# Optimization experiments

Measured on AMD Instinct MI355X. Metric: run time of the kernel, lower is better.

## Reference

```python
import jax, jax.numpy as jnp
import numpy as np

INPUT_SIZE, HIDDEN_SIZE, OUTPUT_SIZE = 64, 256, 1


def setup_inputs() -> dict:
    key = jax.random.key(0)
    ks = jax.random.split(key, 7)
    B, T, I, H, O = 256, 512, INPUT_SIZE, HIDDEN_SIZE, OUTPUT_SIZE
    s_ih = 1.0 / np.sqrt(H)
    return {
        "x": jax.random.normal(ks[0], (B, T, I), dtype=jnp.float32),
        # PyTorch GRUCell layout: rows ordered [reset, update, new], shape [3H, in]
        "w_ih": jax.random.uniform(ks[1], (3 * H, I), jnp.float32, -s_ih, s_ih),
        "w_hh": jax.random.uniform(ks[2], (3 * H, H), jnp.float32, -s_ih, s_ih),
        "b_ih": jax.random.uniform(ks[3], (3 * H,), jnp.float32, -s_ih, s_ih),
        "b_hh": jax.random.uniform(ks[4], (3 * H,), jnp.float32, -s_ih, s_ih),
        "w_out": jax.random.uniform(ks[5], (O, H), jnp.float32, -s_ih, s_ih),
        "b_out": jax.random.uniform(ks[6], (O,), jnp.float32, -s_ih, s_ih),
    }


def reference(x, w_ih, w_hh, b_ih, b_hh, w_out, b_out):
    B, T, I = x.shape
    H = w_hh.shape[1]
    # Precompute all input-side gate projections in one big GEMM: [T, B, 3H]
    gi_all = jnp.einsum("bti,gi->tbg", x, w_ih) + b_ih

    def step(h, gi):
        gh = h @ w_hh.T + b_hh  # [B, 3H]
        i_r, i_z, i_n = jnp.split(gi, 3, axis=-1)
        h_r, h_z, h_n = jnp.split(gh, 3, axis=-1)
        r = jax.nn.sigmoid(i_r + h_r)
        z = jax.nn.sigmoid(i_z + h_z)
        n = jnp.tanh(i_n + r * h_n)
        h_new = (1.0 - z) * n + z * h
        return h_new, h_new

    h0 = jnp.zeros((B, H), dtype=x.dtype)
    _, hs = jax.lax.scan(step, h0, gi_all)  # hs: [T, B, H]
    outs = jnp.einsum("tbh,oh->tbo", hs, w_out) + b_out  # [T, B, O]
    return outs
```

## Files before the change

kernel.cpp:

```cpp
#include <hip/hip_runtime.h>

typedef _Float16 half8 __attribute__((ext_vector_type(8)));
typedef _Float16 f16x2 __attribute__((ext_vector_type(2)));
typedef float floatx4 __attribute__((ext_vector_type(4)));

#define NB 256
#define NT 512
#define NI 64
#define NH 256
#define NSEQ 16
#define NBLK (NB / NSEQ)
#define THR 1024
#define HS 344

#define WB_N (480 * 512)

__global__ __launch_bounds__(256) void gru_prep_kernel(
    const float* __restrict__ w_ih, const float* __restrict__ w_hh,
    _Float16* __restrict__ wb)
{
  int n = blockIdx.x * 256 + threadIdx.x;
  if (n >= WB_N) return;
  int i = n & 7, l = (n >> 3) & 63, f = n >> 9;
  int q = l >> 4, col = l & 15;
  int tt, kb, gate;
  if (f < 160)      { tt = f / 10;               kb = f % 10;        gate = 0; }
  else if (f < 320) { int f2 = f - 160; tt = f2 / 10; kb = f2 % 10;  gate = 1; }
  else if (f < 448) { int f3 = f - 320; tt = f3 / 8;  kb = f3 % 8;   gate = 2; }
  else              { int f4 = f - 448; tt = f4 / 2;  kb = 8 + (f4 & 1); gate = 3; }
  int j = (tt & 15) * 16 + col;
  int k = kb * 32 + q * 8 + i;
  float v;
  if (gate == 0)      v = (k < 256) ? w_hh[(0   + j) * 256 + k] : w_ih[(0   + j) * 64 + (k - 256)];
  else if (gate == 1) v = (k < 256) ? w_hh[(256 + j) * 256 + k] : w_ih[(256 + j) * 64 + (k - 256)];
  else if (gate == 2) v = w_hh[(512 + j) * 256 + k];
  else                v = w_ih[(512 + j) * 64 + (k - 256)];
  wb[n] = (_Float16)v;
}

__device__ __forceinline__ float sigm(float v) {
  return __builtin_amdgcn_rcpf(1.0f + __expf(-v));
}
__device__ __forceinline__ float tanh_f(float v) {
  return 1.0f - 2.0f * __builtin_amdgcn_rcpf(1.0f + __expf(2.0f * v));
}

#define MFMA16(a, b, c) __builtin_amdgcn_mfma_f32_16x16x32_f16(a, b, c, 0, 0, 0)
#define FDOT(W, X, A) __builtin_amdgcn_fdot2(__builtin_bit_cast(f16x2, W), \
                                             __builtin_bit_cast(f16x2, X), A, false)

__global__ __launch_bounds__(THR) void gru_kernel(
    const float* __restrict__ x,
    const float* __restrict__ b_ih,
    const float* __restrict__ b_hh,
    const _Float16* __restrict__ wb,
    _Float16* __restrict__ HD,
    float* __restrict__ out)
{
  __shared__ __align__(16) _Float16 H[2][NSEQ][HS];
  __shared__ __align__(16) _Float16 WN[8 * 16 * 512];

  const int tid  = threadIdx.x;
  const int lane = tid & 63;
  const int w    = tid >> 6;
  const int q    = lane >> 4;
  const int col  = lane & 15;
  const int b0   = blockIdx.x * NSEQ;
  const int j    = w * 16 + col;

  {
    const float4* src = (const float4*)(wb + (size_t)320 * 512);
    float4* dst = (float4*)WN;
    #pragma unroll
    for (int it = 0; it < 8; ++it) dst[tid + it * THR] = src[tid + it * THR];
  }

  const _Float16* wbL = wb + (size_t)lane * 8;
#define LBR(k) const half8 BR##k = *(const half8*)(wbL + (size_t)(w * 10 + (k)) * 512);
  LBR(0) LBR(1) LBR(2) LBR(3) LBR(4) LBR(5) LBR(6) LBR(7) LBR(8) LBR(9)
#undef LBR
#define LBZ(k) const half8 BZ##k = *(const half8*)(wbL + (size_t)(160 + w * 10 + (k)) * 512);
  LBZ(0) LBZ(1) LBZ(2) LBZ(3) LBZ(4) LBZ(5)
#undef LBZ
  const half8* sZ6 = (const half8*)(wbL + (size_t)(160 + w * 10 + 6) * 512);
  const half8* sZ7 = (const half8*)(wbL + (size_t)(160 + w * 10 + 7) * 512);
  const half8* sZ8 = (const half8*)(wbL + (size_t)(160 + w * 10 + 8) * 512);
  const half8* sZ9 = (const half8*)(wbL + (size_t)(160 + w * 10 + 9) * 512);
  const half8* sI0 = (const half8*)(wbL + (size_t)(448 + w * 2 + 0) * 512);
  const half8* sI1 = (const half8*)(wbL + (size_t)(448 + w * 2 + 1) * 512);

  const float br   = b_ih[j] + b_hh[j];
  const float bz   = b_ih[256 + j] + b_hh[256 + j];
  const float bin_ = b_ih[512 + j];
  const float bhn  = b_hh[512 + j];

  {
    float4* hz = (float4*)H;
    #pragma unroll
    for (int it = 0; it < 2; ++it) {
      int idx = tid + it * THR;
      if (idx < (int)(sizeof(H) / 16)) hz[idx] = float4{0, 0, 0, 0};
    }
  }
  __syncthreads();
  H[0][tid >> 6][256 + (tid & 63)] =
      (_Float16)x[(size_t)(b0 + (tid >> 6)) * (NT * NI) + (tid & 63)];
  float h0 = 0.0f, h1 = 0.0f, h2 = 0.0f, h3 = 0.0f;
  const float* xp = x + (size_t)(b0 + (tid >> 6)) * (NT * NI) + 64 + (tid & 63);
  __syncthreads();

  for (int t = 0; t < NT; ++t) {
    const int cur = t & 1, nxt = cur ^ 1;
    half8 SZ6 = *sZ6, SZ7 = *sZ7, SZ8 = *sZ8, SZ9 = *sZ9, SI0i = *sI0, SI1i = *sI1;
    float xv = 0.0f;
    if (t + 1 < NT) xv = xp[(size_t)t * 64];

    if (t > 0 && tid < 512) {
      int row = tid >> 5, ch = tid & 31;
      float4 hv = *(const float4*)&H[cur][row][ch * 8];
      *(float4*)(HD + ((size_t)(t - 1) * NB + b0 + row) * NH + ch * 8) = hv;
    }

    const _Float16* hrow = &H[cur][col][q * 8];
    floatx4 cR = {0, 0, 0, 0}, cZ = {0, 0, 0, 0}, cN = {0, 0, 0, 0}, cI = {0, 0, 0, 0};
#define KBN(k, BZk) { \
    half8 a = *(const half8*)(hrow + (k) * 32); \
    cR = MFMA16(a, BR##k, cR); \
    cZ = MFMA16(a, BZk, cZ); \
    cN = MFMA16(a, *(const half8*)&WN[(w * 8 + (k)) * 512 + lane * 8], cN); }
    KBN(0, BZ0) KBN(1, BZ1) KBN(2, BZ2) KBN(3, BZ3) KBN(4, BZ4) KBN(5, BZ5)
    KBN(6, SZ6) KBN(7, SZ7)
#undef KBN
    { half8 a = *(const half8*)(hrow + 8 * 32);
      cR = MFMA16(a, BR8, cR); cZ = MFMA16(a, SZ8, cZ); cI = MFMA16(a, SI0i, cI); }
    { half8 a = *(const half8*)(hrow + 9 * 32);
      cR = MFMA16(a, BR9, cR); cZ = MFMA16(a, SZ9, cZ); cI = MFMA16(a, SI1i, cI); }

#define GATE(m, hvar) { \
    float rr = sigm(cR[m] + br); \
    float zz = sigm(cZ[m] + bz); \
    float nn = tanh_f(cI[m] + bin_ + rr * (cN[m] + bhn)); \
    hvar = (1.0f - zz) * nn + zz * hvar; \
    H[nxt][q * 4 + (m)][j] = (_Float16)hvar; }
    GATE(0, h0) GATE(1, h1) GATE(2, h2) GATE(3, h3)
#undef GATE
    if (t + 1 < NT) H[nxt][tid >> 6][256 + (tid & 63)] = (_Float16)xv;

    __syncthreads();
  }

  if (tid < 512) {
    int row = tid >> 5, ch = tid & 31;
    float4 hv = *(const float4*)&H[0][row][ch * 8];
    *(float4*)(HD + ((size_t)(NT - 1) * NB + b0 + row) * NH + ch * 8) = hv;
  }
}

__global__ __launch_bounds__(256) void gru_out_kernel(
    const _Float16* __restrict__ HD, const float* __restrict__ w_out,
    const float* __restrict__ b_out, float* __restrict__ out)
{
  __shared__ __align__(16) _Float16 WL[NH];
  int tid = threadIdx.x;
  WL[tid] = (_Float16)w_out[tid];
  __syncthreads();
  int gid = blockIdx.x * 256 + tid;
  const float4* hp = (const float4*)(HD + (size_t)gid * NH);
  const float4* wp = (const float4*)WL;
  float acc = 0.0f;
  #pragma unroll
  for (int i = 0; i < NH / 8; ++i) {
    float4 hv = hp[i];
    float4 wv = wp[i];
    acc = FDOT(hv.x, wv.x, acc);
    acc = FDOT(hv.y, wv.y, acc);
    acc = FDOT(hv.z, wv.z, acc);
    acc = FDOT(hv.w, wv.w, acc);
  }
  out[gid] = acc + b_out[0];
}

extern "C" void kernel_launch(void* const* d_in, const int* in_sizes, int n_in,
                              void* d_out, int out_size, void* d_ws, size_t ws_size,
                              hipStream_t stream) {
  const float* x     = (const float*)d_in[0];
  const float* w_ih  = (const float*)d_in[1];
  const float* w_hh  = (const float*)d_in[2];
  const float* b_ih  = (const float*)d_in[3];
  const float* b_hh  = (const float*)d_in[4];
  const float* w_out = (const float*)d_in[5];
  const float* b_out = (const float*)d_in[6];
  float* out = (float*)d_out;

  _Float16* wb = (_Float16*)d_ws;
  _Float16* HD = wb + WB_N;

  gru_prep_kernel<<<(WB_N + 255) / 256, 256, 0, stream>>>(w_ih, w_hh, wb);
  gru_kernel<<<NBLK, THR, 0, stream>>>(x, b_ih, b_hh, wb, HD, out);
  gru_out_kernel<<<(NT * NB) / 256, 256, 0, stream>>>(HD, w_out, b_out, out);
}
```

Measured before the change: 1.247 ms.

## Halve GRU block to 512 threads, two hidden tiles per wave

Each block now runs 8 waves instead of 16, and each wave computes two 16-column hidden tiles. The R and Z weights for both tiles are held in registers. The N-gate weights are no longer kept in shared memory; they are streamed from global memory each step, with loads interleaved between the MFMA groups and an asm barrier that stops the compiler hoisting them. The aim is to use one A-fragment read from shared memory for twice as many MFMAs and to spend less per step on block barriers, at the cost of much higher register pressure and repeated global or L2 weight loads on every timestep.

```diff
diff --git a/kernel.cpp b/kernel.cpp
--- a/kernel.cpp
+++ b/kernel.cpp
@@ -10,7 +10,7 @@
 #define NH 256
 #define NSEQ 16
 #define NBLK (NB / NSEQ)
-#define THR 1024
+#define THR 512
 #define HS 344
 
 #define WB_N (480 * 512)
@@ -49,7 +49,7 @@
 #define FDOT(W, X, A) __builtin_amdgcn_fdot2(__builtin_bit_cast(f16x2, W), \
                                              __builtin_bit_cast(f16x2, X), A, false)
 
-__global__ __launch_bounds__(THR) void gru_kernel(
+__global__ __launch_bounds__(THR, 2) void gru_kernel(
     const float* __restrict__ x,
     const float* __restrict__ b_ih,
     const float* __restrict__ b_hh,
@@ -58,7 +58,6 @@
     float* __restrict__ out)
 {
   __shared__ __align__(16) _Float16 H[2][NSEQ][HS];
-  __shared__ __align__(16) _Float16 WN[8 * 16 * 512];
 
   const int tid  = threadIdx.x;
   const int lane = tid & 63;
@@ -66,90 +65,123 @@
   const int q    = lane >> 4;
   const int col  = lane & 15;
   const int b0   = blockIdx.x * NSEQ;
-  const int j    = w * 16 + col;
-
-  {
-    const float4* src = (const float4*)(wb + (size_t)320 * 512);
-    float4* dst = (float4*)WN;
-    #pragma unroll
-    for (int it = 0; it < 8; ++it) dst[tid + it * THR] = src[tid + it * THR];
-  }
+  const int t0   = 2 * w;
+  const int t1   = 2 * w + 1;
+  const int j0   = t0 * 16 + col;
+  const int j1   = t1 * 16 + col;
 
   const _Float16* wbL = wb + (size_t)lane * 8;
-#define LBR(k) const half8 BR##k = *(const half8*)(wbL + (size_t)(w * 10 + (k)) * 512);
-  LBR(0) LBR(1) LBR(2) LBR(3) LBR(4) LBR(5) LBR(6) LBR(7) LBR(8) LBR(9)
-#undef LBR
-#define LBZ(k) const half8 BZ##k = *(const half8*)(wbL + (size_t)(160 + w * 10 + (k)) * 512);
-  LBZ(0) LBZ(1) LBZ(2) LBZ(3) LBZ(4) LBZ(5)
-#undef LBZ
-  const half8* sZ6 = (const half8*)(wbL + (size_t)(160 + w * 10 + 6) * 512);
-  const half8* sZ7 = (const half8*)(wbL + (size_t)(160 + w * 10 + 7) * 512);
-  const half8* sZ8 = (const half8*)(wbL + (size_t)(160 + w * 10 + 8) * 512);
-  const half8* sZ9 = (const half8*)(wbL + (size_t)(160 + w * 10 + 9) * 512);
-  const half8* sI0 = (const half8*)(wbL + (size_t)(448 + w * 2 + 0) * 512);
-  const half8* sI1 = (const half8*)(wbL + (size_t)(448 + w * 2 + 1) * 512);
-
-  const float br   = b_ih[j] + b_hh[j];
-  const float bz   = b_ih[256 + j] + b_hh[256 + j];
-  const float bin_ = b_ih[512 + j];
-  const float bhn  = b_hh[512 + j];
+
+#define LR(T, k) const half8 R##T##_##k = *(const half8*)(wbL + (size_t)(t##T * 10 + (k)) * 512);
+  LR(0,0) LR(0,1) LR(0,2) LR(0,3) LR(0,4) LR(0,5) LR(0,6) LR(0,7) LR(0,8) LR(0,9)
+  LR(1,0) LR(1,1) LR(1,2) LR(1,3) LR(1,4) LR(1,5) LR(1,6) LR(1,7) LR(1,8) LR(1,9)
+#undef LR
+#define LZ(T, k) const half8 Z##T##_##k = *(const half8*)(wbL + (size_t)(160 + t##T * 10 + (k)) * 512);
+  LZ(0,0) LZ(0,1) LZ(0,2) LZ(0,3) LZ(0,4) LZ(0,5) LZ(0,6) LZ(0,7) LZ(0,8) LZ(0,9)
+  LZ(1,0) LZ(1,1) LZ(1,2) LZ(1,3) LZ(1,4) LZ(1,5) LZ(1,6) LZ(1,7) LZ(1,8) LZ(1,9)
+#undef LZ
+
+  uintptr_t pN0 = (uintptr_t)(wbL + (size_t)(320 + t0 * 8) * 512);
+  uintptr_t pN1 = (uintptr_t)(wbL + (size_t)(320 + t1 * 8) * 512);
+  uintptr_t pI0 = (uintptr_t)(wbL + (size_t)(448 + t0 * 2) * 512);
+  uintptr_t pI1 = (uintptr_t)(wbL + (size_t)(448 + t1 * 2) * 512);
+
+  const float br0  = b_ih[j0] + b_hh[j0];
+  const float bz0  = b_ih[256 + j0] + b_hh[256 + j0];
+  const float bin0 = b_ih[512 + j0];
+  const float bhn0 = b_hh[512 + j0];
+  const float br1  = b_ih[j1] + b_hh[j1];
+  const float bz1  = b_ih[256 + j1] + b_hh[256 + j1];
+  const float bin1 = b_ih[512 + j1];
+  const float bhn1 = b_hh[512 + j1];
 
   {
     float4* hz = (float4*)H;
     #pragma unroll
-    for (int it = 0; it < 2; ++it) {
+    for (int it = 0; it < 3; ++it) {
       int idx = tid + it * THR;
       if (idx < (int)(sizeof(H) / 16)) hz[idx] = float4{0, 0, 0, 0};
     }
   }
   __syncthreads();
-  H[0][tid >> 6][256 + (tid & 63)] =
-      (_Float16)x[(size_t)(b0 + (tid >> 6)) * (NT * NI) + (tid & 63)];
-  float h0 = 0.0f, h1 = 0.0f, h2 = 0.0f, h3 = 0.0f;
-  const float* xp = x + (size_t)(b0 + (tid >> 6)) * (NT * NI) + 64 + (tid & 63);
+  H[0][w][256 + lane]     = (_Float16)x[(size_t)(b0 + w)     * (NT * NI) + lane];
+  H[0][w + 8][256 + lane] = (_Float16)x[(size_t)(b0 + w + 8) * (NT * NI) + lane];
+  float h00 = 0.0f, h01 = 0.0f, h02 = 0.0f, h03 = 0.0f;
+  float h10 = 0.0f, h11 = 0.0f, h12 = 0.0f, h13 = 0.0f;
+  const float* xp0 = x + (size_t)(b0 + w)     * (NT * NI) + 64 + lane;
+  const float* xp1 = x + (size_t)(b0 + w + 8) * (NT * NI) + 64 + lane;
   __syncthreads();
 
   for (int t = 0; t < NT; ++t) {
     const int cur = t & 1, nxt = cur ^ 1;
-    half8 SZ6 = *sZ6, SZ7 = *sZ7, SZ8 = *sZ8, SZ9 = *sZ9, SI0i = *sI0, SI1i = *sI1;
-    float xv = 0.0f;
-    if (t + 1 < NT) xv = xp[(size_t)t * 64];
-
-    if (t > 0 && tid < 512) {
+    asm("" : "+v"(pN0), "+v"(pN1), "+v"(pI0), "+v"(pI1));
+    const half8* sN0 = (const half8*)pN0;
+    const half8* sN1 = (const half8*)pN1;
+    const half8* sI0 = (const half8*)pI0;
+    const half8* sI1 = (const half8*)pI1;
+
+    half8 sa0 = sN0[0 * 64], sb0 = sN1[0 * 64];
+    half8 sa1 = sN0[1 * 64], sb1 = sN1[1 * 64];
+    half8 sa2 = sN0[2 * 64], sb2 = sN1[2 * 64];
+    float xv0 = 0.0f, xv1 = 0.0f;
+    if (t + 1 < NT) { xv0 = xp0[(size_t)t * 64]; xv1 = xp1[(size_t)t * 64]; }
+
+    if (t > 0) {
       int row = tid >> 5, ch = tid & 31;
       float4 hv = *(const float4*)&H[cur][row][ch * 8];
       *(float4*)(HD + ((size_t)(t - 1) * NB + b0 + row) * NH + ch * 8) = hv;
     }
 
     const _Float16* hrow = &H[cur][col][q * 8];
-    floatx4 cR = {0, 0, 0, 0}, cZ = {0, 0, 0, 0}, cN = {0, 0, 0, 0}, cI = {0, 0, 0, 0};
-#define KBN(k, BZk) { \
+    floatx4 cR0 = {0, 0, 0, 0}, cZ0 = {0, 0, 0, 0}, cN0 = {0, 0, 0, 0}, cI0 = {0, 0, 0, 0};
+    floatx4 cR1 = {0, 0, 0, 0}, cZ1 = {0, 0, 0, 0}, cN1 = {0, 0, 0, 0}, cI1 = {0, 0, 0, 0};
+#define KGRP(k, NA, NB_) { \
     half8 a = *(const half8*)(hrow + (k) * 32); \
-    cR = MFMA16(a, BR##k, cR); \
-    cZ = MFMA16(a, BZk, cZ); \
-    cN = MFMA16(a, *(const half8*)&WN[(w * 8 + (k)) * 512 + lane * 8], cN); }
-    KBN(0, BZ0) KBN(1, BZ1) KBN(2, BZ2) KBN(3, BZ3) KBN(4, BZ4) KBN(5, BZ5)
-    KBN(6, SZ6) KBN(7, SZ7)
-#undef KBN
+    cR0 = MFMA16(a, R0_##k, cR0); cR1 = MFMA16(a, R1_##k, cR1); \
+    cZ0 = MFMA16(a, Z0_##k, cZ0); cZ1 = MFMA16(a, Z1_##k, cZ1); \
+    cN0 = MFMA16(a, NA, cN0);     cN1 = MFMA16(a, NB_, cN1); }
+    KGRP(0, sa0, sb0)  half8 sa3 = sN0[3 * 64], sb3 = sN1[3 * 64];
+    KGRP(1, sa1, sb1)  half8 sa4 = sN0[4 * 64], sb4 = sN1[4 * 64];
+    KGRP(2, sa2, sb2)  half8 sa5 = sN0[5 * 64], sb5 = sN1[5 * 64];
+    KGRP(3, sa3, sb3)  half8 sa6 = sN0[6 * 64], sb6 = sN1[6 * 64];
+    KGRP(4, sa4, sb4)  half8 sa7 = sN0[7 * 64], sb7 = sN1[7 * 64];
+    KGRP(5, sa5, sb5)  half8 ia0 = sI0[0],      ib0 = sI1[0];
+    KGRP(6, sa6, sb6)  half8 ia1 = sI0[64],     ib1 = sI1[64];
+    KGRP(7, sa7, sb7)
+#undef KGRP
     { half8 a = *(const half8*)(hrow + 8 * 32);
-      cR = MFMA16(a, BR8, cR); cZ = MFMA16(a, SZ8, cZ); cI = MFMA16(a, SI0i, cI); }
+      cR0 = MFMA16(a, R0_8, cR0); cR1 = MFMA16(a, R1_8, cR1);
+      cZ0 = MFMA16(a, Z0_8, cZ0); cZ1 = MFMA16(a, Z1_8, cZ1);
+      cI0 = MFMA16(a, ia0, cI0);  cI1 = MFMA16(a, ib0, cI1); }
     { half8 a = *(const half8*)(hrow + 9 * 32);
-      cR = MFMA16(a, BR9, cR); cZ = MFMA16(a, SZ9, cZ); cI = MFMA16(a, SI1i, cI); }
-
-#define GATE(m, hvar) { \
-    float rr = sigm(cR[m] + br); \
-    float zz = sigm(cZ[m] + bz); \
-    float nn = tanh_f(cI[m] + bin_ + rr * (cN[m] + bhn)); \
+      cR0 = MFMA16(a, R0_9, cR0); cR1 = MFMA16(a, R1_9, cR1);
+      cZ0 = MFMA16(a, Z0_9, cZ0); cZ1 = MFMA16(a, Z1_9, cZ1);
+      cI0 = MFMA16(a, ia1, cI0);  cI1 = MFMA16(a, ib1, cI1); }
+
+#define GATE(m, hvar, CR, CZ, CN, CI, BR_, BZ_, BI_, BH_, J) { \
+    float rr = sigm(CR[m] + BR_); \
+    float zz = sigm(CZ[m] + BZ_); \
+    float nn = tanh_f(CI[m] + BI_ + rr * (CN[m] + BH_)); \
     hvar = (1.0f - zz) * nn + zz * hvar; \
-    H[nxt][q * 4 + (m)][j] = (_Float16)hvar; }
-    GATE(0, h0) GATE(1, h1) GATE(2, h2) GATE(3, h3)
+    H[nxt][q * 4 + (m)][J] = (_Float16)hvar; }
+    GATE(0, h00, cR0, cZ0, cN0, cI0, br0, bz0, bin0, bhn0, j0)
+    GATE(1, h01, cR0, cZ0, cN0, cI0, br0, bz0, bin0, bhn0, j0)
+    GATE(2, h02, cR0, cZ0, cN0, cI0, br0, bz0, bin0, bhn0, j0)
+    GATE(3, h03, cR0, cZ0, cN0, cI0, br0, bz0, bin0, bhn0, j0)
+    GATE(0, h10, cR1, cZ1, cN1, cI1, br1, bz1, bin1, bhn1, j1)
+    GATE(1, h11, cR1, cZ1, cN1, cI1, br1, bz1, bin1, bhn1, j1)
+    GATE(2, h12, cR1, cZ1, cN1, cI1, br1, bz1, bin1, bhn1, j1)
+    GATE(3, h13, cR1, cZ1, cN1, cI1, br1, bz1, bin1, bhn1, j1)
 #undef GATE
-    if (t + 1 < NT) H[nxt][tid >> 6][256 + (tid & 63)] = (_Float16)xv;
+    if (t + 1 < NT) {
+      H[nxt][w][256 + lane]     = (_Float16)xv0;
+      H[nxt][w + 8][256 + lane] = (_Float16)xv1;
+    }
 
     __syncthreads();
   }
 
-  if (tid < 512) {
+  {
     int row = tid >> 5, ch = tid & 31;
     float4 hv = *(const float4*)&H[0][row][ch * 8];
     *(float4*)(HD + ((size_t)(NT - 1) * NB + b0 + row) * NH + ch * 8) = hv;
```

Result: slower. 1.615 ms (+29.5%).
